# Kernel optimization log

Measured on AMD Instinct MI355X. Metric: run time of the kernel, lower is better.

The kernel has to match this reference:

```python
import jax, jax.numpy as jnp
import numpy as np

SCALE = 1.0  # alpha / rank = 32 / 32


def setup_inputs() -> dict:
    key = jax.random.key(0)
    k_x, k_w, k_b, k_a, k_bb = jax.random.split(key, 5)
    B, S, D = 4, 4096, 3072
    depth, rank = 4, 32
    x = jax.random.normal(k_x, (B, S, D), dtype=jnp.float32)
    W = jax.random.normal(k_w, (D, D), dtype=jnp.float32) * (1.0 / np.sqrt(D))
    b = jax.random.normal(k_b, (D,), dtype=jnp.float32) * 0.02
    lora_A = jax.random.normal(k_a, (depth, rank, D), dtype=jnp.float32) * (1.0 / np.sqrt(D))
    lora_B = jax.random.normal(k_bb, (depth, D, rank), dtype=jnp.float32) * 0.02
    return {"x": x, "W": W, "b": b, "lora_A": lora_A, "lora_B": lora_B}


def reference(x, W, b, lora_A, lora_B):
    # base: y = x @ W.T + b
    base_out = jnp.einsum('bsi,oi->bso', x, W) + b
    # stacked LoRA: sum_d (x @ A_d.T @ B_d.T); dropout=0 -> identity
    # down-project to rank per depth: [B,S,depth,rank]
    z = jnp.einsum('bsi,dri->bsdr', x, lora_A)
    lora_out = jnp.einsum('bsdr,dor->bso', z, lora_B)
    return base_out + lora_out * SCALE
```

## Files before the change

kernel.cpp:

```cpp
#include <hip/hip_runtime.h>
#include <hip/hip_bf16.h>


typedef unsigned short ushort_t;
typedef short bf16x8 __attribute__((ext_vector_type(8)));
typedef float floatx4 __attribute__((ext_vector_type(4)));
typedef unsigned short ushortx4 __attribute__((ext_vector_type(4)));
typedef unsigned short ushortx8 __attribute__((ext_vector_type(8)));

__device__ __forceinline__ ushort_t f2bf(float f) {
    __hip_bfloat16 h = __float2bfloat16(f);
    return *(ushort_t*)&h;
}

__device__ __forceinline__ void async_load16(const void* g, void* l) {
    __builtin_amdgcn_global_load_lds(
        (const __attribute__((address_space(1))) void*)g,
        (__attribute__((address_space(3))) void*)l,
        16, 0, 0);
}

#define MFMA16(a, b, c) __builtin_amdgcn_mfma_f32_16x16x32_bf16(a, b, c, 0, 0, 0)

__global__ __launch_bounds__(256)
void cvt_kernel(const float* __restrict__ in, ushort_t* __restrict__ out, int n8) {
    int i = blockIdx.x * 256 + threadIdx.x;
    if (i < n8) {
        const float4 v0 = ((const float4*)in)[2 * i];
        const float4 v1 = ((const float4*)in)[2 * i + 1];
        ushortx8 o = { f2bf(v0.x), f2bf(v0.y), f2bf(v0.z), f2bf(v0.w),
                       f2bf(v1.x), f2bf(v1.y), f2bf(v1.z), f2bf(v1.w) };
        ((ushortx8*)out)[i] = o;
    }
}

__global__ __launch_bounds__(256)
void transpose_lora_kernel(const float* __restrict__ lb,
                           const float* __restrict__ la,
                           ushort_t* __restrict__ outB,
                           ushort_t* __restrict__ outA) {
    int bid = blockIdx.x;
    if (bid < 1536) {
        int idx = bid * 256 + threadIdx.x;
        int n = idx >> 7;
        int j = idx & 127;
        int d = j >> 5, r = j & 31;
        outB[idx] = f2bf(lb[(size_t)d * (3072 * 32) + (size_t)n * 32 + r]);
    } else {
        int idx = (bid - 1536) * 256 + threadIdx.x;
        int kk = idx >> 7;
        int j  = idx & 127;
        outA[idx] = f2bf(la[(size_t)j * 3072 + kk]);
    }
}

template <int KT, bool OUT_F32, bool ADD_MAT>
__global__ __launch_bounds__(256)
void gemm_bt_kernel(const ushort_t* __restrict__ A, int lda,
                    const ushort_t* __restrict__ B, int ldb,
                    const float* __restrict__ Cadd,
                    const float* __restrict__ bias,
                    void* __restrict__ Cv, int ldc)
{
    __shared__ ushort_t As[128 * 32];
    __shared__ ushort_t Bs[128 * 32];

    const int t    = threadIdx.x;
    const int lane = t & 63;
    const int wave = t >> 6;
    const int wr   = wave >> 1, wc = wave & 1;
    const int quad = lane >> 4, l16 = lane & 15;

    const int mBase = blockIdx.y * 128;
    const int nBase = blockIdx.x * 128;

    floatx4 acc[4][4] = {};

    const int p0 = t,       r0 = p0 >> 2, g0 = ((p0 & 3) ^ ((r0 >> 1) & 3)) << 3;
    const int p1 = t + 256, r1 = p1 >> 2, g1 = ((p1 & 3) ^ ((r1 >> 1) & 3)) << 3;
    const int qs = (quad ^ ((l16 >> 1) & 3)) << 3;

    for (int kt = 0; kt < KT; ++kt) {
        const int ko = kt * 32;

        async_load16(A + (size_t)(mBase + r0) * lda + ko + g0, &As[p0 * 8]);
        async_load16(A + (size_t)(mBase + r1) * lda + ko + g1, &As[p1 * 8]);
        async_load16(B + (size_t)(nBase + r0) * ldb + ko + g0, &Bs[p0 * 8]);
        async_load16(B + (size_t)(nBase + r1) * ldb + ko + g1, &Bs[p1 * 8]);

        __syncthreads();

        bf16x8 af[4], bf[4];
#pragma unroll
        for (int mi = 0; mi < 4; ++mi)
            af[mi] = *(const bf16x8*)&As[(wr * 64 + mi * 16 + l16) * 32 + qs];
#pragma unroll
        for (int ni = 0; ni < 4; ++ni)
            bf[ni] = *(const bf16x8*)&Bs[(wc * 64 + ni * 16 + l16) * 32 + qs];

#pragma unroll
        for (int mi = 0; mi < 4; ++mi)
#pragma unroll
            for (int ni = 0; ni < 4; ++ni)
                acc[mi][ni] = MFMA16(af[mi], bf[ni], acc[mi][ni]);

        __syncthreads();
    }

#pragma unroll
    for (int ni = 0; ni < 4; ++ni) {
        const int col = nBase + wc * 64 + ni * 16 + l16;
        const float bv = bias ? bias[col] : 0.0f;
#pragma unroll
        for (int mi = 0; mi < 4; ++mi) {
            const int row = mBase + wr * 64 + mi * 16 + quad * 4;
#pragma unroll
            for (int r = 0; r < 4; ++r) {
                float v = acc[mi][ni][r] + bv;
                if (ADD_MAT) v += Cadd[(size_t)(row + r) * ldc + col];
                if (OUT_F32) {
                    ((float*)Cv)[(size_t)(row + r) * ldc + col] = v;
                } else {
                    ((ushort_t*)Cv)[(size_t)(row + r) * ldc + col] = f2bf(v);
                }
            }
        }
    }
}

__global__ __launch_bounds__(512)
void gemm256_kernel(const ushort_t* __restrict__ A,
                    const ushort_t* __restrict__ B,
                    const float* __restrict__ bias,
                    float* __restrict__ C)
{
    constexpr int LDA = 3072;
    constexpr int NT  = 48;
    constexpr int NBX = 12;

    __shared__ ushort_t smem_u[65536];
    char* const smem = (char*)smem_u;

    const int t    = threadIdx.x;
    const int lane = t & 63;
    const int wave = t >> 6;
    const int wr   = wave >> 2;
    const int wc   = wave & 3;
    const int quad = lane >> 4;
    const int l16  = lane & 15;

    const int bid = blockIdx.x;
    const int sw  = (bid & 7) * 96 + (bid >> 3);
    const int bx  = sw % NBX;
    const int by  = sw / NBX;
    const int mBase = by * 256;
    const int nBase = bx * 256;

    const int prow = t >> 3;
    const int cg   = (t & 7) ^ (prow & 7);
    const ushort_t* const aSrc = A + (size_t)(mBase + prow) * LDA + cg * 8;
    const ushort_t* const bSrc = B + (size_t)(nBase + prow) * LDA + cg * 8;
    char* const aDst = smem + t * 16;
    char* const bDst = smem + 32768 + t * 16;

#define STAGE_A(c, h, kt) do {                                              \
        const ushort_t* _s = aSrc + (size_t)(h) * 128 * LDA + (kt) * 64;    \
        char* _d = aDst + (c) * 65536 + (h) * 16384;                        \
        async_load16(_s, _d);                                               \
        async_load16(_s + 64 * LDA, _d + 8192);                             \
    } while (0)
#define STAGE_B(c, h, kt) do {                                              \
        const ushort_t* _s = bSrc + (size_t)(h) * 128 * LDA + (kt) * 64;    \
        char* _d = bDst + (c) * 65536 + (h) * 16384;                        \
        async_load16(_s, _d);                                               \
        async_load16(_s + 64 * LDA, _d + 8192);                             \
    } while (0)

    const int s0  = ((0 + quad) ^ (l16 & 7)) << 4;
    const int s1  = ((4 + quad) ^ (l16 & 7)) << 4;
    const int aRd = wr * 16384 + l16 * 128;
    const int bRd = 32768 + (wc >> 1) * 16384 + ((wc & 1) * 64 + l16) * 128;

    floatx4 acc[8][4] = {};
    bf16x8 af[8][2];
    bf16x8 bfr[2][2];

    STAGE_A(0, 0, 0); STAGE_A(0, 1, 0);
    STAGE_B(0, 0, 0); STAGE_B(0, 1, 0);
    STAGE_A(1, 0, 1); STAGE_A(1, 1, 1);
    STAGE_B(1, 0, 1); STAGE_B(1, 1, 1);
    asm volatile("s_waitcnt vmcnt(8)" ::: "memory");
    __builtin_amdgcn_s_barrier();
    __builtin_amdgcn_sched_barrier(0);

    int cur = 0;
    for (int kt = 0; kt < NT; ++kt) {
        const int cb  = cur << 16;
        const int ktA = (kt + 2 < NT) ? kt + 2 : NT - 1;

#pragma unroll
        for (int mi = 0; mi < 4; ++mi) {
            af[mi][0] = *(const bf16x8*)(smem + cb + aRd + mi * 2048 + s0);
            af[mi][1] = *(const bf16x8*)(smem + cb + aRd + mi * 2048 + s1);
        }
#pragma unroll
        for (int nj = 0; nj < 2; ++nj) {
            bfr[nj][0] = *(const bf16x8*)(smem + cb + bRd + nj * 2048 + s0);
            bfr[nj][1] = *(const bf16x8*)(smem + cb + bRd + nj * 2048 + s1);
        }
        __builtin_amdgcn_s_barrier();
        asm volatile("s_waitcnt lgkmcnt(0)" ::: "memory");
        __builtin_amdgcn_sched_barrier(0);
        __builtin_amdgcn_s_setprio(1);
#pragma unroll
        for (int ks = 0; ks < 2; ++ks)
#pragma unroll
            for (int mi = 0; mi < 4; ++mi)
#pragma unroll
                for (int nj = 0; nj < 2; ++nj)
                    acc[mi][nj] = MFMA16(af[mi][ks], bfr[nj][ks], acc[mi][nj]);
        __builtin_amdgcn_s_setprio(0);
        __builtin_amdgcn_s_barrier();

#pragma unroll
        for (int mi = 4; mi < 8; ++mi) {
            af[mi][0] = *(const bf16x8*)(smem + cb + aRd + mi * 2048 + s0);
            af[mi][1] = *(const bf16x8*)(smem + cb + aRd + mi * 2048 + s1);
        }
        __builtin_amdgcn_s_barrier();
        asm volatile("s_waitcnt lgkmcnt(0)" ::: "memory");
        __builtin_amdgcn_sched_barrier(0);
        __builtin_amdgcn_s_setprio(1);
#pragma unroll
        for (int ks = 0; ks < 2; ++ks)
#pragma unroll
            for (int mi = 4; mi < 8; ++mi)
#pragma unroll
                for (int nj = 0; nj < 2; ++nj)
                    acc[mi][nj] = MFMA16(af[mi][ks], bfr[nj][ks], acc[mi][nj]);
        __builtin_amdgcn_s_setprio(0);
        __builtin_amdgcn_s_barrier();

#pragma unroll
        for (int nj = 0; nj < 2; ++nj) {
            bfr[nj][0] = *(const bf16x8*)(smem + cb + bRd + (2 + nj) * 2048 + s0);
            bfr[nj][1] = *(const bf16x8*)(smem + cb + bRd + (2 + nj) * 2048 + s1);
        }
        STAGE_A(cur, 0, ktA);
        STAGE_A(cur, 1, ktA);
        __builtin_amdgcn_s_barrier();
        asm volatile("s_waitcnt lgkmcnt(0)" ::: "memory");
        __builtin_amdgcn_sched_barrier(0);
        __builtin_amdgcn_s_setprio(1);
#pragma unroll
        for (int ks = 0; ks < 2; ++ks)
#pragma unroll
            for (int mi = 0; mi < 4; ++mi)
#pragma unroll
                for (int nj = 0; nj < 2; ++nj)
                    acc[mi][2 + nj] = MFMA16(af[mi][ks], bfr[nj][ks], acc[mi][2 + nj]);
        __builtin_amdgcn_s_setprio(0);
        __builtin_amdgcn_s_barrier();

        STAGE_B(cur, 0, ktA);
        STAGE_B(cur, 1, ktA);
        __builtin_amdgcn_s_barrier();
        __builtin_amdgcn_sched_barrier(0);
        __builtin_amdgcn_s_setprio(1);
#pragma unroll
        for (int ks = 0; ks < 2; ++ks)
#pragma unroll
            for (int mi = 4; mi < 8; ++mi)
#pragma unroll
                for (int nj = 0; nj < 2; ++nj)
                    acc[mi][2 + nj] = MFMA16(af[mi][ks], bfr[nj][ks], acc[mi][2 + nj]);
        __builtin_amdgcn_s_setprio(0);
        __builtin_amdgcn_sched_barrier(0);
        asm volatile("s_waitcnt vmcnt(8)" ::: "memory");
        __builtin_amdgcn_s_barrier();

        cur ^= 1;
    }

    asm volatile("s_waitcnt vmcnt(0)" ::: "memory");

#pragma unroll
    for (int ni = 0; ni < 4; ++ni) {
        const int col = nBase + wc * 64 + ni * 16 + l16;
        const float bv = bias[col];
#pragma unroll
        for (int mi = 0; mi < 8; ++mi) {
            const int row0 = mBase + wr * 128 + mi * 16 + quad * 4;
            float* cp = C + (size_t)row0 * LDA + col;
#pragma unroll
            for (int r = 0; r < 4; ++r)
                cp[(size_t)r * LDA] = acc[mi][ni][r] + bv;
        }
    }
#undef STAGE_A
#undef STAGE_B
}

extern "C" void kernel_launch(void* const* d_in, const int* in_sizes, int n_in,
                              void* d_out, int out_size, void* d_ws, size_t ws_size,
                              hipStream_t stream) {
    const float* x  = (const float*)d_in[0];
    const float* W  = (const float*)d_in[1];
    const float* b  = (const float*)d_in[2];
    const float* lA = (const float*)d_in[3];
    const float* lB = (const float*)d_in[4];
    float* out = (float*)d_out;

    constexpr int M = 4 * 4096;
    constexpr int N = 3072;
    constexpr int K = 3072;
    constexpr size_t nX  = (size_t)M * K;
    constexpr size_t nW  = (size_t)N * K;
    constexpr size_t nT  = (size_t)128 * K;

    ushort_t* xb    = (ushort_t*)d_ws;
    ushort_t* Weffb = xb + nX;
    ushort_t* Bp    = Weffb + nW;
    ushort_t* At    = Bp + nT;

    cvt_kernel<<<nX / 8 / 256, 256, 0, stream>>>(x, xb, (int)(nX / 8));

    transpose_lora_kernel<<<2 * (nT / 256), 256, 0, stream>>>(lB, lA, Bp, At);

    gemm_bt_kernel<4, false, true><<<dim3(N / 128, N / 128), 256, 0, stream>>>(
        Bp, 128, At, 128, W, nullptr, Weffb, N);

    gemm256_kernel<<<(M / 256) * (N / 256), 512, 0, stream>>>(xb, Weffb, b, out);
}
```

Measured before the change: 670.8 us.

## Triple-buffer B tiles and spread async prefetch issue across phases

Separates the A and B shared-memory buffers and gives B a three-slot ring, with A staying double-buffered, growing LDS from 128KB to 160KB. The next-tile B halves can now be issued at the start of the iteration, and the A and B halves are spread across the four MFMA phases. The intent is to start global loads earlier and hide more load latency behind compute. The cost is more LDS and a changed vmcnt wait placement, which could stall or create hazards if the counts are off.

New measurement: 633.4 us. 1.06x faster.

```diff
diff --git a/kernel.cpp b/kernel.cpp
--- a/kernel.cpp
+++ b/kernel.cpp
@@ -138,7 +138,7 @@
     constexpr int NT  = 48;
     constexpr int NBX = 12;
 
-    __shared__ ushort_t smem_u[65536];
+    __shared__ ushort_t smem_u[81920];
     char* const smem = (char*)smem_u;
 
     const int t    = threadIdx.x;
@@ -160,54 +160,55 @@
     const int cg   = (t & 7) ^ (prow & 7);
     const ushort_t* const aSrc = A + (size_t)(mBase + prow) * LDA + cg * 8;
     const ushort_t* const bSrc = B + (size_t)(nBase + prow) * LDA + cg * 8;
-    char* const aDst = smem + t * 16;
-    char* const bDst = smem + 32768 + t * 16;
-
-#define STAGE_A(c, h, kt) do {                                              \
-        const ushort_t* _s = aSrc + (size_t)(h) * 128 * LDA + (kt) * 64;    \
-        char* _d = aDst + (c) * 65536 + (h) * 16384;                        \
+
+#define STAGE_A(off, h, ktv) do {                                           \
+        const ushort_t* _s = aSrc + (size_t)(h) * 128 * LDA + (ktv) * 64;   \
+        char* _d = smem + (off) + (h) * 16384 + t * 16;                     \
         async_load16(_s, _d);                                               \
         async_load16(_s + 64 * LDA, _d + 8192);                             \
     } while (0)
-#define STAGE_B(c, h, kt) do {                                              \
-        const ushort_t* _s = bSrc + (size_t)(h) * 128 * LDA + (kt) * 64;    \
-        char* _d = bDst + (c) * 65536 + (h) * 16384;                        \
+#define STAGE_B(off, h, ktv) do {                                           \
+        const ushort_t* _s = bSrc + (size_t)(h) * 128 * LDA + (ktv) * 64;   \
+        char* _d = smem + (off) + (h) * 16384 + t * 16;                     \
         async_load16(_s, _d);                                               \
         async_load16(_s + 64 * LDA, _d + 8192);                             \
     } while (0)
 
     const int s0  = ((0 + quad) ^ (l16 & 7)) << 4;
     const int s1  = ((4 + quad) ^ (l16 & 7)) << 4;
-    const int aRd = wr * 16384 + l16 * 128;
-    const int bRd = 32768 + (wc >> 1) * 16384 + ((wc & 1) * 64 + l16) * 128;
+    const int aRdB = wr * 16384 + l16 * 128;
+    const int bRdB = (wc >> 1) * 16384 + ((wc & 1) * 64 + l16) * 128;
 
     floatx4 acc[8][4] = {};
     bf16x8 af[8][2];
     bf16x8 bfr[2][2];
 
-    STAGE_A(0, 0, 0); STAGE_A(0, 1, 0);
-    STAGE_B(0, 0, 0); STAGE_B(0, 1, 0);
-    STAGE_A(1, 0, 1); STAGE_A(1, 1, 1);
-    STAGE_B(1, 0, 1); STAGE_B(1, 1, 1);
+    STAGE_A(0,      0, 0); STAGE_A(0,      1, 0);
+    STAGE_B(65536,  0, 0); STAGE_B(65536,  1, 0);
+    STAGE_A(32768,  0, 1); STAGE_A(32768,  1, 1);
+    STAGE_B(98304,  0, 1); STAGE_B(98304,  1, 1);
     asm volatile("s_waitcnt vmcnt(8)" ::: "memory");
     __builtin_amdgcn_s_barrier();
     __builtin_amdgcn_sched_barrier(0);
 
-    int cur = 0;
+    int aOff = 0;
+    int bRdO = 65536;
+    int bStO = 131072;
+
     for (int kt = 0; kt < NT; ++kt) {
-        const int cb  = cur << 16;
-        const int ktA = (kt + 2 < NT) ? kt + 2 : NT - 1;
+        const int ktN = (kt + 2 < NT) ? kt + 2 : NT - 1;
 
 #pragma unroll
         for (int mi = 0; mi < 4; ++mi) {
-            af[mi][0] = *(const bf16x8*)(smem + cb + aRd + mi * 2048 + s0);
-            af[mi][1] = *(const bf16x8*)(smem + cb + aRd + mi * 2048 + s1);
+            af[mi][0] = *(const bf16x8*)(smem + aOff + aRdB + mi * 2048 + s0);
+            af[mi][1] = *(const bf16x8*)(smem + aOff + aRdB + mi * 2048 + s1);
         }
 #pragma unroll
         for (int nj = 0; nj < 2; ++nj) {
-            bfr[nj][0] = *(const bf16x8*)(smem + cb + bRd + nj * 2048 + s0);
-            bfr[nj][1] = *(const bf16x8*)(smem + cb + bRd + nj * 2048 + s1);
-        }
+            bfr[nj][0] = *(const bf16x8*)(smem + bRdO + bRdB + nj * 2048 + s0);
+            bfr[nj][1] = *(const bf16x8*)(smem + bRdO + bRdB + nj * 2048 + s1);
+        }
+        STAGE_B(bStO, 0, ktN);
         __builtin_amdgcn_s_barrier();
         asm volatile("s_waitcnt lgkmcnt(0)" ::: "memory");
         __builtin_amdgcn_sched_barrier(0);
@@ -224,9 +225,10 @@
 
 #pragma unroll
         for (int mi = 4; mi < 8; ++mi) {
-            af[mi][0] = *(const bf16x8*)(smem + cb + aRd + mi * 2048 + s0);
-            af[mi][1] = *(const bf16x8*)(smem + cb + aRd + mi * 2048 + s1);
-        }
+            af[mi][0] = *(const bf16x8*)(smem + aOff + aRdB + mi * 2048 + s0);
+            af[mi][1] = *(const bf16x8*)(smem + aOff + aRdB + mi * 2048 + s1);
+        }
+        STAGE_B(bStO, 1, ktN);
         __builtin_amdgcn_s_barrier();
         asm volatile("s_waitcnt lgkmcnt(0)" ::: "memory");
         __builtin_amdgcn_sched_barrier(0);
@@ -243,11 +245,10 @@
 
 #pragma unroll
         for (int nj = 0; nj < 2; ++nj) {
-            bfr[nj][0] = *(const bf16x8*)(smem + cb + bRd + (2 + nj) * 2048 + s0);
-            bfr[nj][1] = *(const bf16x8*)(smem + cb + bRd + (2 + nj) * 2048 + s1);
-        }
-        STAGE_A(cur, 0, ktA);
-        STAGE_A(cur, 1, ktA);
+            bfr[nj][0] = *(const bf16x8*)(smem + bRdO + bRdB + (2 + nj) * 2048 + s0);
+            bfr[nj][1] = *(const bf16x8*)(smem + bRdO + bRdB + (2 + nj) * 2048 + s1);
+        }
+        STAGE_A(aOff, 0, ktN);
         __builtin_amdgcn_s_barrier();
         asm volatile("s_waitcnt lgkmcnt(0)" ::: "memory");
         __builtin_amdgcn_sched_barrier(0);
@@ -262,8 +263,8 @@
         __builtin_amdgcn_s_setprio(0);
         __builtin_amdgcn_s_barrier();
 
-        STAGE_B(cur, 0, ktA);
-        STAGE_B(cur, 1, ktA);
+        STAGE_A(aOff, 1, ktN);
+        asm volatile("s_waitcnt vmcnt(8)" ::: "memory");
         __builtin_amdgcn_s_barrier();
         __builtin_amdgcn_sched_barrier(0);
         __builtin_amdgcn_s_setprio(1);
@@ -275,11 +276,11 @@
                 for (int nj = 0; nj < 2; ++nj)
                     acc[mi][2 + nj] = MFMA16(af[mi][ks], bfr[nj][ks], acc[mi][2 + nj]);
         __builtin_amdgcn_s_setprio(0);
-        __builtin_amdgcn_sched_barrier(0);
-        asm volatile("s_waitcnt vmcnt(8)" ::: "memory");
-        __builtin_amdgcn_s_barrier();
-
-        cur ^= 1;
+        __builtin_amdgcn_s_barrier();
+
+        aOff ^= 32768;
+        bRdO = (bRdO == 131072) ? 65536 : bRdO + 32768;
+        bStO = (bStO == 131072) ? 65536 : bStO + 32768;
     }
 
     asm volatile("s_waitcnt vmcnt(0)" ::: "memory");
```
